# Performance work log

Measured on AMD Instinct MI355X. Metric: run time of the kernel, lower is better.

## Reference

```python
import jax, jax.numpy as jnp
import numpy as np
from jax import lax

ANCHOR_BASE = np.array([
    [-37.254833, -82.50967, 53.254833, 98.50967],
    [-82.50967, -173.01933, 98.50967, 189.01933],
    [-173.01933, -354.03867, 189.01933, 370.03867],
    [-56.0, -56.0, 72.0, 72.0],
    [-120.0, -120.0, 136.0, 136.0],
    [-248.0, -248.0, 264.0, 264.0],
    [-82.50967, -37.254833, 98.50967, 53.254833],
    [-173.01933, -82.50967, 189.01933, 98.50967],
    [-354.03867, -173.01933, 370.03867, 189.01933]], dtype=np.float32)
FEAT_STRIDE = 16
IMG_H, IMG_W = 608, 800          # feature map 38x50 at stride 16
NMS_THRESH = 0.7
PRE_NMS, POST_NMS = 6000, 300
MIN_SIZE = 16.0                  # scale = 1.0


def setup_inputs() -> dict:
    key = jax.random.key(0)
    ks = jax.random.split(key, 7)
    H, W = 38, 50
    x = jax.random.normal(ks[0], (1, 512, H, W), jnp.float32)
    conv1_w = jax.random.normal(ks[1], (512, 512, 3, 3), jnp.float32) * 0.01
    conv1_b = jnp.zeros((512,), jnp.float32)
    loc_w = jax.random.normal(ks[2], (36, 512, 1, 1), jnp.float32) * 0.01
    loc_b = jnp.zeros((36,), jnp.float32)
    score_w = jax.random.normal(ks[3], (18, 512, 1, 1), jnp.float32) * 0.01
    score_b = jnp.zeros((18,), jnp.float32)
    return {"x": x, "conv1_w": conv1_w, "conv1_b": conv1_b,
            "loc_w": loc_w, "loc_b": loc_b,
            "score_w": score_w, "score_b": score_b}


def _conv(x, w, b, pad):
    y = lax.conv_general_dilated(x, w, (1, 1), pad,
                                 dimension_numbers=("NCHW", "OIHW", "NCHW"))
    return y + b[None, :, None, None]


def _make_anchors(h, w):
    ab = jnp.asarray(ANCHOR_BASE)                       # [A,4]
    yy = jnp.arange(h, dtype=jnp.float32) * FEAT_STRIDE
    xx = jnp.arange(w, dtype=jnp.float32) * FEAT_STRIDE
    sy, sx = jnp.meshgrid(yy, xx, indexing="ij")        # [h,w]
    shift = jnp.stack([sy, sx, sy, sx], axis=-1).reshape(-1, 4)  # [K,4]
    return (shift[:, None, :] + ab[None, :, :]).reshape(-1, 4)   # [K*A,4]


def _loc2bbox(anchor, loc):
    ah = anchor[:, 2] - anchor[:, 0]
    aw = anchor[:, 3] - anchor[:, 1]
    acy = anchor[:, 0] + 0.5 * ah
    acx = anchor[:, 1] + 0.5 * aw
    dy, dx, dh, dw = loc[:, 0], loc[:, 1], loc[:, 2], loc[:, 3]
    cy = dy * ah + acy
    cx = dx * aw + acx
    h = jnp.exp(dh) * ah
    w = jnp.exp(dw) * aw
    return jnp.stack([cy - 0.5 * h, cx - 0.5 * w,
                      cy + 0.5 * h, cx + 0.5 * w], axis=1)


def _iou_matrix(b):  # b: [K,4] (y1,x1,y2,x2)
    area = (b[:, 2] - b[:, 0]) * (b[:, 3] - b[:, 1])
    ty1 = jnp.maximum(b[:, None, 0], b[None, :, 0])
    tx1 = jnp.maximum(b[:, None, 1], b[None, :, 1])
    ty2 = jnp.minimum(b[:, None, 2], b[None, :, 2])
    tx2 = jnp.minimum(b[:, None, 3], b[None, :, 3])
    inter = jnp.clip(ty2 - ty1, 0) * jnp.clip(tx2 - tx1, 0)
    return inter / jnp.maximum(area[:, None] + area[None, :] - inter, 1e-9)


def _nms_keep(boxes, valid, thresh):
    # boxes already sorted by score desc; greedy suppression.
    K = boxes.shape[0]
    iou = _iou_matrix(boxes)                 # [K,K]
    idx = jnp.arange(K)

    def body(i, keep):
        sup = (iou[i] > thresh) & (idx > i) & keep[i]
        return keep & ~sup

    keep = lax.fori_loop(0, K, body, valid)
    return keep


def reference(x, conv1_w, conv1_b, loc_w, loc_b, score_w, score_b):
    H, W = x.shape[2], x.shape[3]
    A = ANCHOR_BASE.shape[0]

    h1 = jax.nn.relu(_conv(x, conv1_w, conv1_b, ((1, 1), (1, 1))))
    locs = _conv(h1, loc_w, loc_b, ((0, 0), (0, 0)))      # [1,36,H,W]
    scores = _conv(h1, score_w, score_b, ((0, 0), (0, 0)))  # [1,18,H,W]

    locs = locs.transpose(0, 2, 3, 1).reshape(-1, 4)        # [H*W*A,4]
    fg = scores.transpose(0, 2, 3, 1).reshape(H, W, A, 2)[..., 1].reshape(-1)

    anchor = _make_anchors(H, W)
    roi = _loc2bbox(anchor, locs)
    roi = jnp.stack([jnp.clip(roi[:, 0], 0, IMG_H),
                     jnp.clip(roi[:, 1], 0, IMG_W),
                     jnp.clip(roi[:, 2], 0, IMG_H),
                     jnp.clip(roi[:, 3], 0, IMG_W)], axis=1)

    hs = roi[:, 2] - roi[:, 0]
    ws = roi[:, 3] - roi[:, 1]
    valid = (hs >= MIN_SIZE) & (ws >= MIN_SIZE)
    score_f = jnp.where(valid, fg, -jnp.inf)

    top_scores, top_idx = lax.top_k(score_f, PRE_NMS)
    top_boxes = roi[top_idx]                                # [PRE_NMS,4]
    top_valid = top_scores > -jnp.inf

    keep = _nms_keep(top_boxes, top_valid, NMS_THRESH)

    # take first POST_NMS kept boxes into a fixed-shape output
    rank = jnp.cumsum(keep.astype(jnp.int32)) - 1
    dest = jnp.where(keep & (rank < POST_NMS), rank, POST_NMS)
    out = jnp.zeros((POST_NMS + 1, 4), top_boxes.dtype).at[dest].add(top_boxes)
    return out[:POST_NMS]
```

## Files before the change

kernel.cpp:

```cpp
#include <hip/hip_runtime.h>
#include <cstdint>
#include <cstddef>

typedef unsigned long long u64;

#define CIN   512
#define H     38
#define W     50
#define HW    1900
#define PH    40
#define PW    52
#define NA    17100
#define NSORT 32768
#define PRE   6000
#define POST  300
#define NW    94
#define MTS   6016

__constant__ float c_AB[36] = {
  -37.254833f,  -82.50967f,   53.254833f,  98.50967f,
  -82.50967f,  -173.01933f,   98.50967f,  189.01933f,
 -173.01933f,  -354.03867f,  189.01933f,  370.03867f,
  -56.f, -56.f, 72.f, 72.f,
 -120.f,-120.f,136.f,136.f,
 -248.f,-248.f,264.f,264.f,
  -82.50967f,  -37.254833f,   98.50967f,  53.254833f,
 -173.01933f,  -82.50967f,   189.01933f,  98.50967f,
 -354.03867f, -173.01933f,   370.03867f, 189.01933f
};

__global__ __launch_bounds__(256) void pad_kernel(const float* __restrict__ x, float* __restrict__ xp) {
  int idx = blockIdx.x * 256 + threadIdx.x;
  int c   = idx / (PH * PW);
  int rem = idx - c * (PH * PW);
  int yy  = rem / PW;
  int xx  = rem - yy * PW;
  float v = 0.f;
  if (yy >= 1 && yy <= H && xx >= 1 && xx <= W)
    v = x[(size_t)c * HW + (yy - 1) * W + (xx - 1)];
  xp[idx] = v;
}

__global__ __launch_bounds__(256) void wtrans_kernel(const float* __restrict__ w1, float* __restrict__ wt) {
  __shared__ float tile[9][16][17];
  int o0 = blockIdx.x * 16, i0 = blockIdx.y * 16;
  int tx = threadIdx.x & 15, ty = threadIdx.x >> 4;
  #pragma unroll
  for (int r = 0; r < 9; ++r)
    tile[r][tx][ty] = w1[((size_t)(o0 + ty) * CIN + (i0 + tx)) * 9 + r];
  __syncthreads();
  #pragma unroll
  for (int r = 0; r < 9; ++r)
    wt[((size_t)r * CIN + i0 + ty) * CIN + o0 + tx] = tile[r][ty][tx];
}

__global__ __launch_bounds__(256) void wt2prep_kernel(const float* __restrict__ lw, const float* __restrict__ sw,
                                                      float* __restrict__ wt2) {
  int t = blockIdx.x * 256 + threadIdx.x;
  int k = t >> 6, o = t & 63;
  float v = 0.f;
  if (o < 36)      v = lw[o * CIN + k];
  else if (o < 54) v = sw[(o - 36) * CIN + k];
  wt2[t] = v;
}

__global__ __launch_bounds__(256) void conv_gemm_kernel(const float* __restrict__ wt, const float* __restrict__ xp,
                                                        float* __restrict__ part) {
  __shared__ __align__(16) float As[16][64];
  __shared__ __align__(16) float Bs[16][64];
  const int tid   = threadIdx.x;
  const int obase = blockIdx.x * 64;
  const int pbase = blockIdx.y * 64;
  const int split = blockIdx.z;
  const int kbeg = split * 1536, kend = kbeg + 1536;
  const int krow = tid >> 4;
  const int c4   = (tid & 15) * 4;
  const int to   = (tid & 15) * 4;
  const int tp   = (tid >> 4) * 4;
  float acc[4][4] = {};
  float av[4], bv[4];

  auto loadAB = [&](int k0) {
    int k = k0 + krow;
    const float* ap = &wt[(size_t)k * CIN + obase + c4];
    av[0] = ap[0]; av[1] = ap[1]; av[2] = ap[2]; av[3] = ap[3];
    int r = k >> 9;
    int i = k & 511;
    int ky = r / 3, kx = r - ky * 3;
    const float* xpi = &xp[(size_t)i * (PH * PW)];
    #pragma unroll
    for (int j = 0; j < 4; ++j) {
      int p = pbase + c4 + j;
      float v = 0.f;
      if (p < HW) {
        int y = p / W, xx = p - y * W;
        v = xpi[(y + ky) * PW + xx + kx];
      }
      bv[j] = v;
    }
  };

  loadAB(kbeg);
  for (int k0 = kbeg; k0 < kend; k0 += 16) {
    __syncthreads();
    *(float4*)&As[krow][c4] = make_float4(av[0], av[1], av[2], av[3]);
    *(float4*)&Bs[krow][c4] = make_float4(bv[0], bv[1], bv[2], bv[3]);
    __syncthreads();
    if (k0 + 16 < kend) loadAB(k0 + 16);
    #pragma unroll
    for (int kk = 0; kk < 16; ++kk) {
      float4 a4 = *(const float4*)&As[kk][to];
      float4 b4 = *(const float4*)&Bs[kk][tp];
      float ar[4] = {a4.x, a4.y, a4.z, a4.w};
      float br[4] = {b4.x, b4.y, b4.z, b4.w};
      #pragma unroll
      for (int ii = 0; ii < 4; ++ii)
        #pragma unroll
        for (int jj = 0; jj < 4; ++jj)
          acc[ii][jj] += ar[ii] * br[jj];
    }
  }
  float* dst = part + (size_t)split * CIN * HW;
  #pragma unroll
  for (int ii = 0; ii < 4; ++ii) {
    int o = obase + to + ii;
    int p = pbase + tp;
    float* rowp = dst + (size_t)o * HW;
    if (p + 3 < HW) {
      *(float4*)&rowp[p] = make_float4(acc[ii][0], acc[ii][1], acc[ii][2], acc[ii][3]);
    } else {
      #pragma unroll
      for (int jj = 0; jj < 4; ++jj) if (p + jj < HW) rowp[p + jj] = acc[ii][jj];
    }
  }
}

__global__ __launch_bounds__(256) void reduce_relu_kernel(const float* __restrict__ part, const float* __restrict__ b1,
                                                          float* __restrict__ h1) {
  int idx = blockIdx.x * 256 + threadIdx.x;
  int o = idx / HW;
  float v = part[idx] + part[(size_t)CIN * HW + idx] + part[(size_t)2 * CIN * HW + idx] + b1[o];
  h1[idx] = v > 0.f ? v : 0.f;
}

__global__ __launch_bounds__(256) void heads_gemm_kernel(const float* __restrict__ wt2, const float* __restrict__ h1,
                                                         const float* __restrict__ lb, const float* __restrict__ sb,
                                                         float* __restrict__ c2) {
  __shared__ __align__(16) float As[16][64];
  __shared__ __align__(16) float Bs[16][64];
  const int tid   = threadIdx.x;
  const int pbase = blockIdx.x * 64;
  const int krow = tid >> 4;
  const int c4   = (tid & 15) * 4;
  const int to   = (tid & 15) * 4;
  const int tp   = (tid >> 4) * 4;
  float acc[4][4] = {};
  float av[4], bv[4];

  auto loadAB = [&](int k0) {
    int k = k0 + krow;
    const float4 a4 = *(const float4*)&wt2[k * 64 + c4];
    av[0] = a4.x; av[1] = a4.y; av[2] = a4.z; av[3] = a4.w;
    #pragma unroll
    for (int j = 0; j < 4; ++j) {
      int p = pbase + c4 + j;
      bv[j] = (p < HW) ? h1[(size_t)k * HW + p] : 0.f;
    }
  };

  loadAB(0);
  for (int k0 = 0; k0 < CIN; k0 += 16) {
    __syncthreads();
    *(float4*)&As[krow][c4] = make_float4(av[0], av[1], av[2], av[3]);
    *(float4*)&Bs[krow][c4] = make_float4(bv[0], bv[1], bv[2], bv[3]);
    __syncthreads();
    if (k0 + 16 < CIN) loadAB(k0 + 16);
    #pragma unroll
    for (int kk = 0; kk < 16; ++kk) {
      float4 a4 = *(const float4*)&As[kk][to];
      float4 b4 = *(const float4*)&Bs[kk][tp];
      float ar[4] = {a4.x, a4.y, a4.z, a4.w};
      float br[4] = {b4.x, b4.y, b4.z, b4.w};
      #pragma unroll
      for (int ii = 0; ii < 4; ++ii)
        #pragma unroll
        for (int jj = 0; jj < 4; ++jj)
          acc[ii][jj] += ar[ii] * br[jj];
    }
  }
  #pragma unroll
  for (int ii = 0; ii < 4; ++ii) {
    int o = to + ii;
    float bias = 0.f;
    if (o < 36) bias = lb[o]; else if (o < 54) bias = sb[o - 36];
    int p = pbase + tp;
    float* rowp = c2 + (size_t)o * HW;
    #pragma unroll
    for (int jj = 0; jj < 4; ++jj) if (p + jj < HW) rowp[p + jj] = acc[ii][jj] + bias;
  }
}

__global__ __launch_bounds__(256) void decode_kernel(const float* __restrict__ c2, float* __restrict__ roi,
                                                     u64* __restrict__ keys) {
  int n = blockIdx.x * 256 + threadIdx.x;
  if (n >= NSORT) return;
  if (n >= NA) { keys[n] = ~0ull; return; }
  unsigned p = (unsigned)n / 9u;
  unsigned a = (unsigned)n - p * 9u;
  unsigned y = p / 50u;
  unsigned x = p - y * 50u;
  float dy = c2[(a * 4 + 0) * HW + p];
  float dx = c2[(a * 4 + 1) * HW + p];
  float dh = c2[(a * 4 + 2) * HW + p];
  float dw = c2[(a * 4 + 3) * HW + p];
  float fg = c2[(37 + a * 2) * HW + p];
  float sy = (float)(y * 16u), sx = (float)(x * 16u);
  float ay1 = sy + c_AB[a * 4 + 0], ax1 = sx + c_AB[a * 4 + 1];
  float ay2 = sy + c_AB[a * 4 + 2], ax2 = sx + c_AB[a * 4 + 3];
  float ahh = ay2 - ay1, aww = ax2 - ax1;
  float acy = ay1 + 0.5f * ahh, acx = ax1 + 0.5f * aww;
  float cy = dy * ahh + acy, cx = dx * aww + acx;
  float hh = expf(dh) * ahh, ww = expf(dw) * aww;
  float y1 = cy - 0.5f * hh, x1 = cx - 0.5f * ww;
  float y2 = cy + 0.5f * hh, x2 = cx + 0.5f * ww;
  y1 = fminf(fmaxf(y1, 0.f), 608.f); x1 = fminf(fmaxf(x1, 0.f), 800.f);
  y2 = fminf(fmaxf(y2, 0.f), 608.f); x2 = fminf(fmaxf(x2, 0.f), 800.f);
  *(float4*)&roi[(size_t)n * 4] = make_float4(y1, x1, y2, x2);
  bool valid = ((y2 - y1) >= 16.f) && ((x2 - x1) >= 16.f);
  float sc = valid ? fg : -__builtin_huge_valf();
  unsigned m = __float_as_uint(sc);
  m = (m & 0x80000000u) ? ~m : (m | 0x80000000u);
  unsigned km = ~m;
  keys[n] = ((u64)km << 32) | (unsigned)n;
}

__global__ __launch_bounds__(1024) void sort_kernel(u64* __restrict__ keys) {
  __shared__ u64 s[8192];
  const int tid = threadIdx.x;
  u64* base = keys + (size_t)blockIdx.x * 8192;
  for (int i = tid; i < 8192; i += 1024) s[i] = base[i];
  __syncthreads();
  for (int k = 2; k <= 8192; k <<= 1) {
    for (int j = k >> 1; j > 0; j >>= 1) {
      for (int i = tid; i < 8192; i += 1024) {
        int l = i ^ j;
        if (l > i) {
          u64 xa = s[i], xb = s[l];
          bool up = ((i & k) == 0);
          if ((xa > xb) == up) { s[i] = xb; s[l] = xa; }
        }
      }
      __syncthreads();
    }
  }
  for (int i = tid; i < 8192; i += 1024) base[i] = s[i];
}

__device__ inline void merge_path(const u64* __restrict__ A, int nA, const u64* __restrict__ B, int nB,
                                  u64* __restrict__ dst, int d0, int cnt, int outLimit) {
  if (d0 >= outLimit || d0 >= nA + nB) return;
  int lo = d0 > nB ? d0 - nB : 0;
  int hi = d0 < nA ? d0 : nA;
  while (lo < hi) {
    int mid = (lo + hi) >> 1;
    if (A[mid] <= B[d0 - 1 - mid]) lo = mid + 1; else hi = mid;
  }
  int i = lo, j = d0 - lo;
  int end = d0 + cnt;
  if (end > nA + nB) end = nA + nB;
  if (end > outLimit) end = outLimit;
  for (int q = d0; q < end; ++q) {
    u64 v;
    if (i < nA && (j >= nB || A[i] <= B[j])) v = A[i++]; else v = B[j++];
    dst[q] = v;
  }
}
__global__ __launch_bounds__(256) void merge1_kernel(const u64* __restrict__ keys, u64* __restrict__ tmp) {
  int pair = blockIdx.y;
  int gid = blockIdx.x * 256 + threadIdx.x;
  const u64* A = keys + (size_t)pair * 16384;
  merge_path(A, 8192, A + 8192, 8192, tmp + (size_t)pair * 16384, gid * 16, 16, 16384);
}
__global__ __launch_bounds__(256) void merge2_kernel(const u64* __restrict__ tmp, u64* __restrict__ topk) {
  int gid = blockIdx.x * 256 + threadIdx.x;
  merge_path(tmp, 16384, tmp + 16384, 16384, topk, gid * 16, 16, 6016);
}

__global__ __launch_bounds__(256) void gather_kernel(const u64* __restrict__ topk, const float* __restrict__ roi,
                                                     float* __restrict__ tb, float* __restrict__ areaArr,
                                                     u64* __restrict__ valw) {
  int j = blockIdx.x * 256 + threadIdx.x;
  u64 key = (j < 6016) ? topk[j] : ~0ull;
  bool valid = (j < PRE) && ((unsigned)(key >> 32) < 0xFF800000u);
  if (j < PRE) {
    unsigned idx = (unsigned)key;
    float4 b = *(const float4*)&roi[(size_t)idx * 4];
    *(float4*)&tb[(size_t)j * 4] = b;
    areaArr[j] = (b.z - b.x) * (b.w - b.y);
  }
  u64 mask = __ballot(valid);
  if ((threadIdx.x & 63) == 0) {
    int wi = j >> 6;
    if (wi < NW) valw[wi] = mask;
  }
}

__global__ __launch_bounds__(256) void mask_kernel(const float* __restrict__ tb, const float* __restrict__ areaArr,
                                                   u64* __restrict__ MT) {
  int linear = blockIdx.x * 256 + threadIdx.x;
  if (linear >= NW * PRE) return;
  int w = linear / PRE;
  int i = linear - w * PRE;
  u64 bits = 0;
  int jbase = w * 64;
  if (jbase + 63 > i) {
    float4 bi = *(const float4*)&tb[(size_t)i * 4];
    float ai = areaArr[i];
    int jend = jbase + 64; if (jend > PRE) jend = PRE;
    int jst = jbase > i + 1 ? jbase : i + 1;
    for (int j = jst; j < jend; ++j) {
      float4 bj = *(const float4*)&tb[(size_t)j * 4];
      float ty1 = fmaxf(bi.x, bj.x);
      float tx1 = fmaxf(bi.y, bj.y);
      float ty2 = fminf(bi.z, bj.z);
      float tx2 = fminf(bi.w, bj.w);
      float ih = ty2 - ty1; if (ih < 0.f) ih = 0.f;
      float iw = tx2 - tx1; if (iw < 0.f) iw = 0.f;
      float inter = ih * iw;
      float denom = ai + areaArr[j] - inter;
      if (denom < 1e-9f) denom = 1e-9f;
      if (inter / denom > 0.7f) bits |= (1ull << (j - jbase));
    }
  }
  MT[(size_t)w * MTS + i] = bits;
}

__device__ inline u64 shfl_u64(u64 v, int src) {
  int lo = __shfl((int)(unsigned)(v & 0xffffffffull), src, 64);
  int hi = __shfl((int)(unsigned)(v >> 32), src, 64);
  return ((u64)(unsigned)hi << 32) | (unsigned)lo;
}

__global__ __launch_bounds__(64) void nms_scan_kernel(const u64* __restrict__ MT, const u64* __restrict__ valw,
                                                      const float* __restrict__ tb, float* __restrict__ out) {
  __shared__ u64 removed[NW];
  __shared__ int keepids[POST];
  const int lane = threadIdx.x;
  for (int wk = lane; wk < NW; wk += 64) removed[wk] = 0;
  __syncthreads();
  int kept = 0;
  bool done = false;
  for (int g = 0; g < NW && !done; ++g) {
    int row = g * 64 + lane;
    u64 cur = (row < PRE) ? MT[(size_t)g * MTS + row] : 0ull;
    u64 v = valw[g];
    u64 r = removed[g];
    u64 kb = 0;
    u64 remaining = v & ~r;
    while (remaining) {
      int c = __builtin_ctzll(remaining);
      if (lane == 0) keepids[kept] = g * 64 + c;
      kb |= (1ull << c);
      ++kept;
      if (kept >= POST) { done = true; break; }
      u64 cw = shfl_u64(cur, c);
      r |= cw;
      u64 above = (c == 63) ? 0ull : (~0ull << (c + 1));
      remaining = v & ~r & above;
    }
    if (!done) {
      __syncthreads();
      for (int wk = g + 1 + lane; wk < NW; wk += 64) {
        u64 acc2 = removed[wk];
        u64 m = kb;
        while (m) {
          int b = __builtin_ctzll(m); m &= m - 1;
          acc2 |= MT[(size_t)wk * MTS + g * 64 + b];
        }
        removed[wk] = acc2;
      }
      __syncthreads();
    }
  }
  __syncthreads();
  int kmax = kept < POST ? kept : POST;
  for (int rr = lane; rr < kmax; rr += 64) {
    float4 b = *(const float4*)&tb[(size_t)keepids[rr] * 4];
    *(float4*)&out[(size_t)rr * 4] = b;
  }
}

extern "C" void kernel_launch(void* const* d_in, const int* in_sizes, int n_in,
                              void* d_out, int out_size, void* d_ws, size_t ws_size,
                              hipStream_t stream) {
  (void)in_sizes; (void)n_in; (void)ws_size;
  const float* x  = (const float*)d_in[0];
  const float* w1 = (const float*)d_in[1];
  const float* b1 = (const float*)d_in[2];
  const float* lw = (const float*)d_in[3];
  const float* lb = (const float*)d_in[4];
  const float* sw = (const float*)d_in[5];
  const float* sb = (const float*)d_in[6];
  float* out = (float*)d_out;

  char* wp = (char*)d_ws;
  auto alloc = [&](size_t b) -> void* { void* p = wp; wp += (b + 255) & ~(size_t)255; return p; };
  float* xp      = (float*)alloc((size_t)CIN * PH * PW * 4);
  float* wt      = (float*)alloc((size_t)4608 * CIN * 4);
  float* part    = (float*)alloc((size_t)3 * CIN * HW * 4);
  float* h1      = (float*)alloc((size_t)CIN * HW * 4);
  float* wt2     = (float*)alloc((size_t)CIN * 64 * 4);
  float* c2      = (float*)alloc((size_t)64 * HW * 4);
  float* roi     = (float*)alloc((size_t)NA * 4 * 4);
  u64*   keys    = (u64*)alloc((size_t)NSORT * 8);
  u64*   tmp     = (u64*)alloc((size_t)NSORT * 8);
  u64*   topk    = (u64*)alloc((size_t)8192 * 8);
  float* tb      = (float*)alloc((size_t)PRE * 4 * 4);
  float* areaArr = (float*)alloc((size_t)PRE * 4);
  u64*   valw    = (u64*)alloc((size_t)NW * 8);
  u64*   MT      = (u64*)alloc((size_t)NW * MTS * 8);

  hipMemsetAsync(d_out, 0, (size_t)out_size * 4, stream);

  pad_kernel<<<(CIN * PH * PW) / 256, 256, 0, stream>>>(x, xp);
  wtrans_kernel<<<dim3(32, 32), 256, 0, stream>>>(w1, wt);
  wt2prep_kernel<<<(CIN * 64) / 256, 256, 0, stream>>>(lw, sw, wt2);
  conv_gemm_kernel<<<dim3(8, 30, 3), 256, 0, stream>>>(wt, xp, part);
  reduce_relu_kernel<<<(CIN * HW) / 256, 256, 0, stream>>>(part, b1, h1);
  heads_gemm_kernel<<<30, 256, 0, stream>>>(wt2, h1, lb, sb, c2);
  decode_kernel<<<NSORT / 256, 256, 0, stream>>>(c2, roi, keys);
  sort_kernel<<<4, 1024, 0, stream>>>(keys);
  merge1_kernel<<<dim3(4, 2), 256, 0, stream>>>(keys, tmp);
  merge2_kernel<<<2, 256, 0, stream>>>(tmp, topk);
  gather_kernel<<<24, 256, 0, stream>>>(topk, roi, tb, areaArr, valw);
  mask_kernel<<<(NW * PRE + 255) / 256, 256, 0, stream>>>(tb, areaArr, MT);
  nms_scan_kernel<<<1, 64, 0, stream>>>(MT, valw, tb, out);
}
```

Before: 560.1 us.

## Use 8x8 register micro-tiles with 64-thread blocks in conv GEMM

New measurement: 609.4 us. 1.09x slower.

```diff
diff --git a/kernel.cpp b/kernel.cpp
--- a/kernel.cpp
+++ b/kernel.cpp
@@ -64,74 +64,91 @@
   wt2[t] = v;
 }
 
-__global__ __launch_bounds__(256) void conv_gemm_kernel(const float* __restrict__ wt, const float* __restrict__ xp,
-                                                        float* __restrict__ part) {
+__global__ __launch_bounds__(64) void conv_gemm_kernel(const float* __restrict__ wt, const float* __restrict__ xp,
+                                                       float* __restrict__ part) {
   __shared__ __align__(16) float As[16][64];
   __shared__ __align__(16) float Bs[16][64];
-  const int tid   = threadIdx.x;
+  const int t     = threadIdx.x;
   const int obase = blockIdx.x * 64;
   const int pbase = blockIdx.y * 64;
   const int split = blockIdx.z;
-  const int kbeg = split * 1536, kend = kbeg + 1536;
-  const int krow = tid >> 4;
-  const int c4   = (tid & 15) * 4;
-  const int to   = (tid & 15) * 4;
-  const int tp   = (tid >> 4) * 4;
-  float acc[4][4] = {};
-  float av[4], bv[4];
+  const int kbeg  = split * 1536, kend = kbeg + 1536;
+  const int rbase = t >> 4;
+  const int cq    = t & 15;
+  const int to    = (t & 7) * 8;
+  const int tp    = (t >> 3) * 8;
+
+  const int p0 = pbase + cq * 4;
+  const bool pv = (p0 < HW);
+  unsigned yq = (unsigned)p0 / 50u;
+  int xq = p0 - (int)yq * 50;
+  int boff[4];
+  #pragma unroll
+  for (int e = 0; e < 4; ++e) {
+    int xe = xq + e;
+    int ye = (int)yq + (xe >= 50 ? 1 : 0);
+    if (xe >= 50) xe -= 50;
+    boff[e] = ye * PW + xe;
+  }
+
+  float acc[8][8] = {};
+  float av[16], bv[16];
 
   auto loadAB = [&](int k0) {
-    int k = k0 + krow;
-    const float* ap = &wt[(size_t)k * CIN + obase + c4];
-    av[0] = ap[0]; av[1] = ap[1]; av[2] = ap[2]; av[3] = ap[3];
-    int r = k >> 9;
-    int i = k & 511;
-    int ky = r / 3, kx = r - ky * 3;
-    const float* xpi = &xp[(size_t)i * (PH * PW)];
     #pragma unroll
     for (int j = 0; j < 4; ++j) {
-      int p = pbase + c4 + j;
-      float v = 0.f;
-      if (p < HW) {
-        int y = p / W, xx = p - y * W;
-        v = xpi[(y + ky) * PW + xx + kx];
+      int k = k0 + rbase + 4 * j;
+      const float4 a4 = *(const float4*)&wt[(size_t)k * CIN + obase + cq * 4];
+      av[4*j+0] = a4.x; av[4*j+1] = a4.y; av[4*j+2] = a4.z; av[4*j+3] = a4.w;
+      unsigned r = (unsigned)k >> 9;
+      int i = k & 511;
+      unsigned ky = r / 3u;
+      int kx = (int)(r - ky * 3u);
+      const float* xb = xp + (size_t)i * (PH * PW) + (int)ky * PW + kx;
+      if (pv) {
+        bv[4*j+0] = xb[boff[0]]; bv[4*j+1] = xb[boff[1]];
+        bv[4*j+2] = xb[boff[2]]; bv[4*j+3] = xb[boff[3]];
+      } else {
+        bv[4*j+0] = 0.f; bv[4*j+1] = 0.f; bv[4*j+2] = 0.f; bv[4*j+3] = 0.f;
       }
-      bv[j] = v;
     }
   };
 
   loadAB(kbeg);
   for (int k0 = kbeg; k0 < kend; k0 += 16) {
     __syncthreads();
-    *(float4*)&As[krow][c4] = make_float4(av[0], av[1], av[2], av[3]);
-    *(float4*)&Bs[krow][c4] = make_float4(bv[0], bv[1], bv[2], bv[3]);
+    #pragma unroll
+    for (int j = 0; j < 4; ++j) {
+      *(float4*)&As[rbase + 4*j][cq*4] = make_float4(av[4*j+0], av[4*j+1], av[4*j+2], av[4*j+3]);
+      *(float4*)&Bs[rbase + 4*j][cq*4] = make_float4(bv[4*j+0], bv[4*j+1], bv[4*j+2], bv[4*j+3]);
+    }
     __syncthreads();
     if (k0 + 16 < kend) loadAB(k0 + 16);
     #pragma unroll
     for (int kk = 0; kk < 16; ++kk) {
-      float4 a4 = *(const float4*)&As[kk][to];
-      float4 b4 = *(const float4*)&Bs[kk][tp];
-      float ar[4] = {a4.x, a4.y, a4.z, a4.w};
-      float br[4] = {b4.x, b4.y, b4.z, b4.w};
+      float4 a0 = *(const float4*)&As[kk][to];
+      float4 a1 = *(const float4*)&As[kk][to + 4];
+      float4 b0 = *(const float4*)&Bs[kk][tp];
+      float4 b1 = *(const float4*)&Bs[kk][tp + 4];
+      float ar[8] = {a0.x, a0.y, a0.z, a0.w, a1.x, a1.y, a1.z, a1.w};
+      float br[8] = {b0.x, b0.y, b0.z, b0.w, b1.x, b1.y, b1.z, b1.w};
       #pragma unroll
-      for (int ii = 0; ii < 4; ++ii)
+      for (int ii = 0; ii < 8; ++ii)
         #pragma unroll
-        for (int jj = 0; jj < 4; ++jj)
+        for (int jj = 0; jj < 8; ++jj)
           acc[ii][jj] += ar[ii] * br[jj];
     }
   }
+
   float* dst = part + (size_t)split * CIN * HW;
   #pragma unroll
-  for (int ii = 0; ii < 4; ++ii) {
-    int o = obase + to + ii;
+  for (int ii = 0; ii < 8; ++ii) {
+    float* rowp = dst + (size_t)(obase + to + ii) * HW;
     int p = pbase + tp;
-    float* rowp = dst + (size_t)o * HW;
-    if (p + 3 < HW) {
-      *(float4*)&rowp[p] = make_float4(acc[ii][0], acc[ii][1], acc[ii][2], acc[ii][3]);
-    } else {
-      #pragma unroll
-      for (int jj = 0; jj < 4; ++jj) if (p + jj < HW) rowp[p + jj] = acc[ii][jj];
-    }
+    if (p < HW)
+      *(float4*)&rowp[p]     = make_float4(acc[ii][0], acc[ii][1], acc[ii][2], acc[ii][3]);
+    if (p + 4 < HW)
+      *(float4*)&rowp[p + 4] = make_float4(acc[ii][4], acc[ii][5], acc[ii][6], acc[ii][7]);
   }
 }
 
@@ -425,7 +442,7 @@
   pad_kernel<<<(CIN * PH * PW) / 256, 256, 0, stream>>>(x, xp);
   wtrans_kernel<<<dim3(32, 32), 256, 0, stream>>>(w1, wt);
   wt2prep_kernel<<<(CIN * 64) / 256, 256, 0, stream>>>(lw, sw, wt2);
-  conv_gemm_kernel<<<dim3(8, 30, 3), 256, 0, stream>>>(wt, xp, part);
+  conv_gemm_kernel<<<dim3(8, 30, 3), 64, 0, stream>>>(wt, xp, part);
   reduce_relu_kernel<<<(CIN * HW) / 256, 256, 0, stream>>>(part, b1, h1);
   heads_gemm_kernel<<<30, 256, 0, stream>>>(wt2, h1, lb, sb, c2);
   decode_kernel<<<NSORT / 256, 256, 0, stream>>>(c2, roi, keys);
```

## Replace shared-memory tiled conv GEMM with direct register-pipelined global loads

Applied to the files above, without the earlier changes.

Result: slower. 697.8 us (+24.6%).

```diff
diff --git a/kernel.cpp b/kernel.cpp
--- a/kernel.cpp
+++ b/kernel.cpp
@@ -66,53 +66,63 @@
 
 __global__ __launch_bounds__(256) void conv_gemm_kernel(const float* __restrict__ wt, const float* __restrict__ xp,
                                                         float* __restrict__ part) {
-  __shared__ __align__(16) float As[16][64];
-  __shared__ __align__(16) float Bs[16][64];
-  const int tid   = threadIdx.x;
+  const int t     = threadIdx.x;
   const int obase = blockIdx.x * 64;
   const int pbase = blockIdx.y * 64;
-  const int split = blockIdx.z;
-  const int kbeg = split * 1536, kend = kbeg + 1536;
-  const int krow = tid >> 4;
-  const int c4   = (tid & 15) * 4;
-  const int to   = (tid & 15) * 4;
-  const int tp   = (tid >> 4) * 4;
+  const int ky    = blockIdx.z;
+  const int kbeg  = ky * 1536;
+  const int to    = (t & 15) * 4;
+  const int tp    = (t >> 4) * 4;
+  const int aoff  = obase + to;
+
+  int p0 = pbase + tp;
+  if (p0 >= HW) p0 = 0;
+  const int y0 = p0 / 50;
+  const int x0 = p0 - y0 * 50;
+  int boff[4];
+  #pragma unroll
+  for (int e = 0; e < 4; ++e) {
+    int xe = x0 + e, ye = y0;
+    if (xe >= 50) { xe -= 50; ye += 1; }
+    boff[e] = ye * PW + xe;
+  }
+
   float acc[4][4] = {};
-  float av[4], bv[4];
-
-  auto loadAB = [&](int k0) {
-    int k = k0 + krow;
-    const float* ap = &wt[(size_t)k * CIN + obase + c4];
-    av[0] = ap[0]; av[1] = ap[1]; av[2] = ap[2]; av[3] = ap[3];
-    int r = k >> 9;
-    int i = k & 511;
-    int ky = r / 3, kx = r - ky * 3;
-    const float* xpi = &xp[(size_t)i * (PH * PW)];
+
+  for (int kx = 0; kx < 3; ++kx) {
+    const float* __restrict__ ab = wt + (size_t)(kbeg + kx * 512) * CIN;
+    const float* __restrict__ bb = xp + ky * PW + kx;
+
+    float4 a[8];
+    float  b[8][4];
     #pragma unroll
-    for (int j = 0; j < 4; ++j) {
-      int p = pbase + c4 + j;
-      float v = 0.f;
-      if (p < HW) {
-        int y = p / W, xx = p - y * W;
-        v = xpi[(y + ky) * PW + xx + kx];
+    for (int j = 0; j < 8; ++j) {
+      a[j] = *(const float4*)(ab + (size_t)j * CIN + aoff);
+      const float* bi = bb + (size_t)j * (PH * PW);
+      b[j][0] = bi[boff[0]]; b[j][1] = bi[boff[1]];
+      b[j][2] = bi[boff[2]]; b[j][3] = bi[boff[3]];
+    }
+    for (int i = 0; i < 512 - 8; i += 8) {
+      #pragma unroll
+      for (int j = 0; j < 8; ++j) {
+        float ar[4] = {a[j].x, a[j].y, a[j].z, a[j].w};
+        float br[4] = {b[j][0], b[j][1], b[j][2], b[j][3]};
+        #pragma unroll
+        for (int ii = 0; ii < 4; ++ii)
+          #pragma unroll
+          for (int jj = 0; jj < 4; ++jj)
+            acc[ii][jj] += ar[ii] * br[jj];
+        const int i2 = i + 8 + j;
+        a[j] = *(const float4*)(ab + (size_t)i2 * CIN + aoff);
+        const float* bi = bb + (size_t)i2 * (PH * PW);
+        b[j][0] = bi[boff[0]]; b[j][1] = bi[boff[1]];
+        b[j][2] = bi[boff[2]]; b[j][3] = bi[boff[3]];
       }
-      bv[j] = v;
-    }
-  };
-
-  loadAB(kbeg);
-  for (int k0 = kbeg; k0 < kend; k0 += 16) {
-    __syncthreads();
-    *(float4*)&As[krow][c4] = make_float4(av[0], av[1], av[2], av[3]);
-    *(float4*)&Bs[krow][c4] = make_float4(bv[0], bv[1], bv[2], bv[3]);
-    __syncthreads();
-    if (k0 + 16 < kend) loadAB(k0 + 16);
+    }
     #pragma unroll
-    for (int kk = 0; kk < 16; ++kk) {
-      float4 a4 = *(const float4*)&As[kk][to];
-      float4 b4 = *(const float4*)&Bs[kk][tp];
-      float ar[4] = {a4.x, a4.y, a4.z, a4.w};
-      float br[4] = {b4.x, b4.y, b4.z, b4.w};
+    for (int j = 0; j < 8; ++j) {
+      float ar[4] = {a[j].x, a[j].y, a[j].z, a[j].w};
+      float br[4] = {b[j][0], b[j][1], b[j][2], b[j][3]};
       #pragma unroll
       for (int ii = 0; ii < 4; ++ii)
         #pragma unroll
@@ -120,7 +130,8 @@
           acc[ii][jj] += ar[ii] * br[jj];
     }
   }
-  float* dst = part + (size_t)split * CIN * HW;
+
+  float* dst = part + (size_t)ky * CIN * HW;
   #pragma unroll
   for (int ii = 0; ii < 4; ++ii) {
     int o = obase + to + ii;
```

## Split top-k sort into smaller chunk sorts and truncated shared-memory merges

Applied to the files above, without the earlier changes.

After: 527.7 us. -5.8%, faster.

```diff
diff --git a/kernel.cpp b/kernel.cpp
--- a/kernel.cpp
+++ b/kernel.cpp
@@ -16,6 +16,7 @@
 #define POST  300
 #define NW    94
 #define MTS   6016
+#define TOPN  6016
 
 __constant__ float c_AB[36] = {
   -37.254833f,  -82.50967f,   53.254833f,  98.50967f,
@@ -234,15 +235,15 @@
   keys[n] = ((u64)km << 32) | (unsigned)n;
 }
 
-__global__ __launch_bounds__(1024) void sort_kernel(u64* __restrict__ keys) {
-  __shared__ u64 s[8192];
+__global__ __launch_bounds__(256) void sortchunk_kernel(u64* __restrict__ keys) {
+  __shared__ u64 s[2048];
   const int tid = threadIdx.x;
-  u64* base = keys + (size_t)blockIdx.x * 8192;
-  for (int i = tid; i < 8192; i += 1024) s[i] = base[i];
-  __syncthreads();
-  for (int k = 2; k <= 8192; k <<= 1) {
+  u64* base = keys + (size_t)blockIdx.x * 2048;
+  for (int i = tid; i < 2048; i += 256) s[i] = base[i];
+  __syncthreads();
+  for (int k = 2; k <= 2048; k <<= 1) {
     for (int j = k >> 1; j > 0; j >>= 1) {
-      for (int i = tid; i < 8192; i += 1024) {
+      for (int i = tid; i < 2048; i += 256) {
         int l = i ^ j;
         if (l > i) {
           u64 xa = s[i], xb = s[l];
@@ -253,7 +254,7 @@
       __syncthreads();
     }
   }
-  for (int i = tid; i < 8192; i += 1024) base[i] = s[i];
+  for (int i = tid; i < 2048; i += 256) base[i] = s[i];
 }
 
 __device__ inline void merge_path(const u64* __restrict__ A, int nA, const u64* __restrict__ B, int nB,
@@ -275,22 +276,33 @@
     dst[q] = v;
   }
 }
-__global__ __launch_bounds__(256) void merge1_kernel(const u64* __restrict__ keys, u64* __restrict__ tmp) {
-  int pair = blockIdx.y;
-  int gid = blockIdx.x * 256 + threadIdx.x;
-  const u64* A = keys + (size_t)pair * 16384;
-  merge_path(A, 8192, A + 8192, 8192, tmp + (size_t)pair * 16384, gid * 16, 16, 16384);
-}
-__global__ __launch_bounds__(256) void merge2_kernel(const u64* __restrict__ tmp, u64* __restrict__ topk) {
-  int gid = blockIdx.x * 256 + threadIdx.x;
-  merge_path(tmp, 16384, tmp + 16384, 16384, topk, gid * 16, 16, 6016);
+
+__global__ __launch_bounds__(256) void merge4_kernel(const u64* __restrict__ keys, u64* __restrict__ tmp) {
+  __shared__ u64 M01[4096];
+  __shared__ u64 M23[4096];
+  const int tid = threadIdx.x;
+  const u64* c = keys + (size_t)blockIdx.x * 8192;
+  merge_path(c,        2048, c + 2048, 2048, M01, tid * 16, 16, 4096);
+  merge_path(c + 4096, 2048, c + 6144, 2048, M23, tid * 16, 16, 4096);
+  __syncthreads();
+  merge_path(M01, 4096, M23, 4096, tmp + (size_t)blockIdx.x * TOPN, tid * 24, 24, TOPN);
+}
+
+__global__ __launch_bounds__(256) void mergefinal_kernel(const u64* __restrict__ tmp, u64* __restrict__ topk) {
+  __shared__ u64 L0[TOPN];
+  __shared__ u64 L1[TOPN];
+  const int tid = threadIdx.x;
+  merge_path(tmp,            TOPN, tmp + TOPN,     TOPN, L0, tid * 24, 24, TOPN);
+  merge_path(tmp + 2 * TOPN, TOPN, tmp + 3 * TOPN, TOPN, L1, tid * 24, 24, TOPN);
+  __syncthreads();
+  merge_path(L0, TOPN, L1, TOPN, topk, tid * 24, 24, TOPN);
 }
 
 __global__ __launch_bounds__(256) void gather_kernel(const u64* __restrict__ topk, const float* __restrict__ roi,
                                                      float* __restrict__ tb, float* __restrict__ areaArr,
                                                      u64* __restrict__ valw) {
   int j = blockIdx.x * 256 + threadIdx.x;
-  u64 key = (j < 6016) ? topk[j] : ~0ull;
+  u64 key = (j < TOPN) ? topk[j] : ~0ull;
   bool valid = (j < PRE) && ((unsigned)(key >> 32) < 0xFF800000u);
   if (j < PRE) {
     unsigned idx = (unsigned)key;
@@ -429,9 +441,9 @@
   reduce_relu_kernel<<<(CIN * HW) / 256, 256, 0, stream>>>(part, b1, h1);
   heads_gemm_kernel<<<30, 256, 0, stream>>>(wt2, h1, lb, sb, c2);
   decode_kernel<<<NSORT / 256, 256, 0, stream>>>(c2, roi, keys);
-  sort_kernel<<<4, 1024, 0, stream>>>(keys);
-  merge1_kernel<<<dim3(4, 2), 256, 0, stream>>>(keys, tmp);
-  merge2_kernel<<<2, 256, 0, stream>>>(tmp, topk);
+  sortchunk_kernel<<<16, 256, 0, stream>>>(keys);
+  merge4_kernel<<<4, 256, 0, stream>>>(keys, tmp);
+  mergefinal_kernel<<<1, 256, 0, stream>>>(tmp, topk);
   gather_kernel<<<24, 256, 0, stream>>>(topk, roi, tb, areaArr, valw);
   mask_kernel<<<(NW * PRE + 255) / 256, 256, 0, stream>>>(tb, areaArr, MT);
   nms_scan_kernel<<<1, 64, 0, stream>>>(MT, valw, tb, out);
```
